# Kernel tuning notes

Hardware: AMD Instinct MI355X
Metric: run time of the kernel (lower is better)

The kernel has to match this reference:

```python
import jax, jax.numpy as jnp
import numpy as np

# my_conv from Sufficient-Vision-Transformer: unfold + per-channel weighted sums
# over k*k patch positions (two weight sets), concat, interleave channels, add bias.
# This is exactly a depthwise conv with 2 filters per input channel, output
# channels interleaved as [res1_0, res2_0, res1_1, res2_1, ...].

K = 3       # kernel_size
PAD = 1     # padding
STRIDE = 1  # stride


def setup_inputs() -> dict:
    key = jax.random.key(0)
    k1, k2, k3, k4 = jax.random.split(key, 4)
    B, C, H, W = 32, 192, 56, 56
    x = jax.random.normal(k1, (B, C, H, W), dtype=jnp.float32)
    weight1 = jax.random.normal(k2, (1, 1, C, K * K), dtype=jnp.float32)
    weight2 = jax.random.normal(k3, (1, 1, C, K * K), dtype=jnp.float32)
    bias = jax.random.normal(k4, (1, 2 * C, 1, 1), dtype=jnp.float32)
    return {"x": x, "weight1": weight1, "weight2": weight2, "bias": bias}


def reference(x, weight1, weight2, bias):
    B, C, H, W = x.shape
    # torch Unfold orders patch rows channel-major, kernel positions row-major
    # (kh, kw) -> matches reshape of weight (C, k*k) -> (C, 1, k, k).
    w1 = weight1.reshape(C, 1, K, K)
    w2 = weight2.reshape(C, 1, K, K)
    # Interleave filters per group: group i -> output channels [2i, 2i+1]
    # with feature_group_count=C; reproduces order_list = [0, C, 1, C+1, ...].
    w = jnp.stack([w1, w2], axis=1).reshape(2 * C, 1, K, K)
    out = jax.lax.conv_general_dilated(
        x, w,
        window_strides=(STRIDE, STRIDE),
        padding=[(PAD, PAD), (PAD, PAD)],
        feature_group_count=C,
        dimension_numbers=("NCHW", "OIHW", "NCHW"),
    )
    return out + bias
```

## Files before the change

### kernel.cpp

```cpp
#include <hip/hip_runtime.h>


#define BB 32
#define CC 192
#define HH 56
#define WW 56
#define W4 14
#define PITCH 60
#define LROWS 58

typedef float f32x4 __attribute__((ext_vector_type(4)));

__global__ __launch_bounds__(784) void dwconv2_lds_kernel(
    const float* __restrict__ x,
    const float* __restrict__ w1,
    const float* __restrict__ w2,
    const float* __restrict__ bias,
    float* __restrict__ out)
{
    __shared__ float tile[LROWS * PITCH];
    __shared__ float wts[20];

    const int bc = blockIdx.x;
    const int c  = bc % CC;

    const int t  = threadIdx.x;
    const int h  = t / W4;
    const int w4 = t % W4;
    const int w0 = w4 * 4;

    if (t < 9)        wts[t]      = w1[c * 9 + t];
    else if (t < 18)  wts[t]      = w2[c * 9 + (t - 9)];
    else if (t < 20)  wts[t]      = bias[2 * c + (t - 18)];

    if (t < 60)            tile[t] = 0.f;
    else if (t < 120)      tile[57 * PITCH + (t - 60)] = 0.f;
    else if (t < 176)      tile[(t - 119) * PITCH] = 0.f;
    else if (t < 232)      tile[(t - 175) * PITCH + 57] = 0.f;

    const f32x4 v = __builtin_nontemporal_load(
        (const f32x4*)(x + ((size_t)bc * HH + h) * WW + w0));
    float* dst = &tile[(h + 1) * PITCH + 1 + w0];
    dst[0] = v.x; dst[1] = v.y; dst[2] = v.z; dst[3] = v.w;

    __syncthreads();

    float a1[9], a2[9];
#pragma unroll
    for (int i = 0; i < 9; ++i) { a1[i] = wts[i]; a2[i] = wts[9 + i]; }
    const float bias1 = wts[18], bias2 = wts[19];

    float o1[4], o2[4];
#pragma unroll
    for (int p = 0; p < 4; ++p) { o1[p] = bias1; o2[p] = bias2; }

#pragma unroll
    for (int r = 0; r < 3; ++r) {
        const float* rp = &tile[(h + r) * PITCH + w0];
        float rv[6];
#pragma unroll
        for (int j = 0; j < 6; ++j) rv[j] = rp[j];
#pragma unroll
        for (int p = 0; p < 4; ++p) {
#pragma unroll
            for (int kc = 0; kc < 3; ++kc) {
                o1[p] += rv[p + kc] * a1[r * 3 + kc];
                o2[p] += rv[p + kc] * a2[r * 3 + kc];
            }
        }
    }

    const size_t obase = (((size_t)(bc * 2) * HH) + h) * WW + w0;
    f32x4 s1; s1.x = o1[0]; s1.y = o1[1]; s1.z = o1[2]; s1.w = o1[3];
    f32x4 s2; s2.x = o2[0]; s2.y = o2[1]; s2.z = o2[2]; s2.w = o2[3];
    __builtin_nontemporal_store(s1, (f32x4*)(out + obase));
    __builtin_nontemporal_store(s2, (f32x4*)(out + obase + (size_t)HH * WW));
}

extern "C" void kernel_launch(void* const* d_in, const int* in_sizes, int n_in,
                              void* d_out, int out_size, void* d_ws, size_t ws_size,
                              hipStream_t stream) {
    const float* x  = (const float*)d_in[0];
    const float* w1 = (const float*)d_in[1];
    const float* w2 = (const float*)d_in[2];
    const float* bs = (const float*)d_in[3];
    float* out = (float*)d_out;

    dwconv2_lds_kernel<<<BB * CC, 784, 0, stream>>>(x, w1, w2, bs, out);
}
```

Baseline: 239.1 us.

## Replace LDS tile with register sliding window over row strips

```diff
diff --git a/kernel.cpp b/kernel.cpp
--- a/kernel.cpp
+++ b/kernel.cpp
@@ -1,80 +1,94 @@
 #include <hip/hip_runtime.h>
 
 
-#define BB 32
 #define CC 192
 #define HH 56
 #define WW 56
 #define W4 14
-#define PITCH 60
-#define LROWS 58
+#define STRIPS 4
+#define RPS 14
+#define PPB 8
+#define TPB (PPB * 56)
 
 typedef float f32x4 __attribute__((ext_vector_type(4)));
 
-__global__ __launch_bounds__(784) void dwconv2_lds_kernel(
+__global__ __launch_bounds__(TPB) void dwconv2_reg_kernel(
     const float* __restrict__ x,
     const float* __restrict__ w1,
     const float* __restrict__ w2,
     const float* __restrict__ bias,
     float* __restrict__ out)
 {
-    __shared__ float tile[LROWS * PITCH];
-    __shared__ float wts[20];
-
-    const int bc = blockIdx.x;
-    const int c  = bc % CC;
-
-    const int t  = threadIdx.x;
-    const int h  = t / W4;
-    const int w4 = t % W4;
-    const int w0 = w4 * 4;
-
-    if (t < 9)        wts[t]      = w1[c * 9 + t];
-    else if (t < 18)  wts[t]      = w2[c * 9 + (t - 9)];
-    else if (t < 20)  wts[t]      = bias[2 * c + (t - 18)];
-
-    if (t < 60)            tile[t] = 0.f;
-    else if (t < 120)      tile[57 * PITCH + (t - 60)] = 0.f;
-    else if (t < 176)      tile[(t - 119) * PITCH] = 0.f;
-    else if (t < 232)      tile[(t - 175) * PITCH + 57] = 0.f;
-
-    const f32x4 v = __builtin_nontemporal_load(
-        (const f32x4*)(x + ((size_t)bc * HH + h) * WW + w0));
-    float* dst = &tile[(h + 1) * PITCH + 1 + w0];
-    dst[0] = v.x; dst[1] = v.y; dst[2] = v.z; dst[3] = v.w;
-
-    __syncthreads();
+    const int t     = threadIdx.x;
+    const int w4    = t % W4;
+    const int strip = (t / W4) % STRIPS;
+    const int pl    = t / 56;
+    const int bc    = blockIdx.x * PPB + pl;
+    const int c     = bc % CC;
 
     float a1[9], a2[9];
 #pragma unroll
-    for (int i = 0; i < 9; ++i) { a1[i] = wts[i]; a2[i] = wts[9 + i]; }
-    const float bias1 = wts[18], bias2 = wts[19];
+    for (int i = 0; i < 9; ++i) { a1[i] = w1[c * 9 + i]; a2[i] = w2[c * 9 + i]; }
+    const float b1 = bias[2 * c];
+    const float b2 = bias[2 * c + 1];
 
-    float o1[4], o2[4];
-#pragma unroll
-    for (int p = 0; p < 4; ++p) { o1[p] = bias1; o2[p] = bias2; }
+    const int h0 = strip * RPS;
+    const int w0 = w4 * 4;
+    const float* xp = x + (size_t)bc * HH * WW + w0;
+    float* op1 = out + (((size_t)bc * 2) * HH + h0) * WW + w0;
+    float* op2 = op1 + (size_t)HH * WW;
+
+    const bool has_left  = (w0 > 0);
+    const bool has_right = (w0 + 4 < WW);
+
+    float r[3][6];
+
+#define LOAD_ROW(hh, dst)                                                    \
+    do {                                                                     \
+        const int _hh = (hh);                                                \
+        const bool _hv = (_hh >= 0) && (_hh < HH);                           \
+        const float* _rp = xp + (size_t)_hh * WW;                            \
+        f32x4 _v = {0.f, 0.f, 0.f, 0.f};                                     \
+        if (_hv) _v = *(const f32x4*)_rp;                                    \
+        (dst)[0] = (_hv && has_left)  ? _rp[-1] : 0.f;                       \
+        (dst)[1] = _v.x; (dst)[2] = _v.y; (dst)[3] = _v.z; (dst)[4] = _v.w;  \
+        (dst)[5] = (_hv && has_right) ? _rp[4]  : 0.f;                       \
+    } while (0)
+
+    LOAD_ROW(h0 - 1, r[0]);
+    LOAD_ROW(h0,     r[1]);
 
 #pragma unroll
-    for (int r = 0; r < 3; ++r) {
-        const float* rp = &tile[(h + r) * PITCH + w0];
-        float rv[6];
+    for (int j = 0; j < RPS; ++j) {
+        LOAD_ROW(h0 + j + 1, r[(j + 2) % 3]);
+
+        const float* top = r[(j + 0) % 3];
+        const float* mid = r[(j + 1) % 3];
+        const float* bot = r[(j + 2) % 3];
+
+        float o1v[4], o2v[4];
 #pragma unroll
-        for (int j = 0; j < 6; ++j) rv[j] = rp[j];
+        for (int p = 0; p < 4; ++p) { o1v[p] = b1; o2v[p] = b2; }
+
 #pragma unroll
         for (int p = 0; p < 4; ++p) {
 #pragma unroll
             for (int kc = 0; kc < 3; ++kc) {
-                o1[p] += rv[p + kc] * a1[r * 3 + kc];
-                o2[p] += rv[p + kc] * a2[r * 3 + kc];
+                o1v[p] += top[p + kc] * a1[0 + kc];
+                o1v[p] += mid[p + kc] * a1[3 + kc];
+                o1v[p] += bot[p + kc] * a1[6 + kc];
+                o2v[p] += top[p + kc] * a2[0 + kc];
+                o2v[p] += mid[p + kc] * a2[3 + kc];
+                o2v[p] += bot[p + kc] * a2[6 + kc];
             }
         }
+
+        f32x4 s1; s1.x = o1v[0]; s1.y = o1v[1]; s1.z = o1v[2]; s1.w = o1v[3];
+        f32x4 s2; s2.x = o2v[0]; s2.y = o2v[1]; s2.z = o2v[2]; s2.w = o2v[3];
+        __builtin_nontemporal_store(s1, (f32x4*)(op1 + (size_t)j * WW));
+        __builtin_nontemporal_store(s2, (f32x4*)(op2 + (size_t)j * WW));
     }
-
-    const size_t obase = (((size_t)(bc * 2) * HH) + h) * WW + w0;
-    f32x4 s1; s1.x = o1[0]; s1.y = o1[1]; s1.z = o1[2]; s1.w = o1[3];
-    f32x4 s2; s2.x = o2[0]; s2.y = o2[1]; s2.z = o2[2]; s2.w = o2[3];
-    __builtin_nontemporal_store(s1, (f32x4*)(out + obase));
-    __builtin_nontemporal_store(s2, (f32x4*)(out + obase + (size_t)HH * WW));
+#undef LOAD_ROW
 }
 
 extern "C" void kernel_launch(void* const* d_in, const int* in_sizes, int n_in,
@@ -86,5 +100,7 @@
     const float* bs = (const float*)d_in[3];
     float* out = (float*)d_out;
 
-    dwconv2_lds_kernel<<<BB * CC, 784, 0, stream>>>(x, w1, w2, bs, out);
+    const int planes = 32 * CC;
+    const int grid = planes / PPB;
+    dwconv2_reg_kernel<<<grid, TPB, 0, stream>>>(x, w1, w2, bs, out);
 }
```

Result: slower. 253.7 us (+6.1%).
